# Optimization experiments

Hardware: AMD Instinct MI355X
Metric: run time of the kernel (lower is better)

## Reference

```python
import jax, jax.numpy as jnp
import numpy as np

H = 768
NH = 12
HD = H // NH


def setup_inputs() -> dict:
    key = jax.random.key(0)
    ks = jax.random.split(key, 12)
    B, S = 2, 2048
    s = 1.0 / np.sqrt(H)
    inp = {
        "hidden_states": jax.random.normal(ks[0], (B, S, H), dtype=jnp.float32),
        "attention_mask": jnp.ones((B, S), dtype=jnp.float32),
        "Wq": jax.random.normal(ks[1], (H, H), dtype=jnp.float32) * s,
        "bq": jnp.zeros((H,), dtype=jnp.float32),
        "Wk": jax.random.normal(ks[2], (H, H), dtype=jnp.float32) * s,
        "bk": jnp.zeros((H,), dtype=jnp.float32),
        "Wv": jax.random.normal(ks[3], (H, H), dtype=jnp.float32) * s,
        "bv": jnp.zeros((H,), dtype=jnp.float32),
        "Wo": jax.random.normal(ks[4], (H, H), dtype=jnp.float32) * s,
        "bo": jnp.zeros((H,), dtype=jnp.float32),
        "ln_gamma": jnp.ones((H,), dtype=jnp.float32),
        "ln_beta": jnp.zeros((H,), dtype=jnp.float32),
    }
    return inp


def _split_heads(x):
    # [B,S,H] -> [B,NH,S,HD]
    B, S, _ = x.shape
    return x.reshape(B, S, NH, HD).transpose(0, 2, 1, 3)


def reference(hidden_states, attention_mask, Wq, bq, Wk, bk, Wv, bv, Wo, bo, ln_gamma, ln_beta):
    x = hidden_states
    q = _split_heads(x @ Wq.T + bq)
    k = _split_heads(x @ Wk.T + bk)
    v = _split_heads(x @ Wv.T + bv)
    # scores: [B,NH,S,S]
    scores = jnp.einsum("bhqd,bhkd->bhqk", q, k) / jnp.sqrt(jnp.float32(HD))
    mask = (1.0 - attention_mask)[:, None, None, :] * -10000.0
    scores = scores + mask
    probs = jax.nn.softmax(scores, axis=-1)  # dropout is identity at inference
    ctx = jnp.einsum("bhqk,bhkd->bhqd", probs, v)
    B, _, S, _ = ctx.shape
    ctx = ctx.transpose(0, 2, 1, 3).reshape(B, S, H)
    out = ctx @ Wo.T + bo
    y = out + x
    mu = jnp.mean(y, axis=-1, keepdims=True)
    var = jnp.var(y, axis=-1, keepdims=True)
    y = (y - mu) / jnp.sqrt(var + 1e-5)
    return y * ln_gamma + ln_beta
```

## Files before the change

### kernel.cpp

```cpp
#include <hip/hip_runtime.h>
#include <math.h>

#define HH 768
#define NHEADS 12
#define HDIM 64
#define SEQ 2048
#define NB 2
#define L2E 1.44269504088896f

typedef __attribute__((ext_vector_type(8))) short s8v;
typedef __attribute__((ext_vector_type(4))) short s4v;
typedef __attribute__((ext_vector_type(4))) float f4v;

static __device__ inline short f2bf(float f) {
    union { float f; unsigned u; } v; v.f = f;
    unsigned r = v.u + 0x7fff + ((v.u >> 16) & 1);
    return (short)(r >> 16);
}

#if __has_builtin(__builtin_amdgcn_exp2f)
#define EXP2(x) __builtin_amdgcn_exp2f(x)
#else
#define EXP2(x) __expf((x) * 0.6931471805599453f)
#endif

__device__ __forceinline__ unsigned cvt_pk_bf16(float a, float b) {
    unsigned r;
    asm("v_cvt_pk_bf16_f32 %0, %1, %2" : "=v"(r) : "v"(a), "v"(b));
    return r;
}

__device__ __forceinline__ void gld16(const void* g, void* l) {
    __builtin_amdgcn_global_load_lds(
        (const __attribute__((address_space(1))) void*)g,
        (__attribute__((address_space(3))) void*)l, 16, 0, 0);
}

__device__ __forceinline__ int kperm(int k) {
    return (k & ~31) | (((k >> 2) & 3) << 3) | (((k >> 4) & 1) << 2) | (k & 3);
}

#define XV8   393216
#define WV8   73728
__global__ __launch_bounds__(256)
void cvt_kernel(const float* __restrict__ X, short* __restrict__ Xb,
                const float* __restrict__ W0, short* __restrict__ W0b,
                const float* __restrict__ W1, short* __restrict__ W1b,
                const float* __restrict__ W2, short* __restrict__ W2b,
                const float* __restrict__ W3, short* __restrict__ W3b)
{
    int gid = blockIdx.x * 256 + threadIdx.x;
    const float* src; short* dst; size_t off;
    if      (gid < XV8)            { src = X;  dst = Xb;  off = gid; }
    else if (gid < XV8 + WV8)      { src = W0; dst = W0b; off = gid - XV8; }
    else if (gid < XV8 + 2*WV8)    { src = W1; dst = W1b; off = gid - XV8 - WV8; }
    else if (gid < XV8 + 3*WV8)    { src = W2; dst = W2b; off = gid - XV8 - 2*WV8; }
    else if (gid < XV8 + 4*WV8)    { src = W3; dst = W3b; off = gid - XV8 - 3*WV8; }
    else return;
    off *= 8;
    float4 a = *(const float4*)(src + off);
    float4 b = *(const float4*)(src + off + 4);
    s8v o;
    o[0] = f2bf(a.x); o[1] = f2bf(a.y); o[2] = f2bf(a.z); o[3] = f2bf(a.w);
    o[4] = f2bf(b.x); o[5] = f2bf(b.y); o[6] = f2bf(b.z); o[7] = f2bf(b.w);
    *(s8v*)(dst + off) = o;
}

#define NKT (HH/32)
template<int EPI>
__global__ __launch_bounds__(256)
void gemm_mfma(const short* __restrict__ A,
               const short* __restrict__ Wq, const short* __restrict__ Wk,
               const short* __restrict__ Wv,
               const float* __restrict__ bq, const float* __restrict__ bk,
               const float* __restrict__ bv,
               short* __restrict__ Qo, short* __restrict__ Ko, short* __restrict__ Vo,
               const float* __restrict__ Xres, float* __restrict__ Fo)
{
    __shared__ __align__(16) short As[3*64*32];
    __shared__ __align__(16) short Bs[3*128*32];

    const int tid  = threadIdx.x;
    const int w    = tid >> 6;
    const int lane = tid & 63;
    const int g    = lane >> 4;
    const int r    = lane & 15;
    const int wr   = w >> 1;
    const int wc   = w & 1;

    const int NBX = (EPI == 0) ? 18 : 6;
    const int NXB = (EPI == 0) ? 144 : 48;
    const int wg  = (blockIdx.x & 7) * NXB + (blockIdx.x >> 3);
    const int bx  = wg % NBX;
    const int by  = wg / NBX;
    const int m0  = by * 64;

    int n0;
    int seg = 0;
    const short* Wb; const float* bias; short* outp; float scale;
    if (EPI == 0) {
        seg = bx / 6;
        n0 = (bx % 6) * 128;
        Wb   = seg == 0 ? Wq : seg == 1 ? Wk : Wv;
        bias = seg == 0 ? bq : seg == 1 ? bk : bv;
        outp = seg == 0 ? Qo : seg == 1 ? Ko : Vo;
        scale = seg == 0 ? (0.125f * L2E) : 1.0f;
    } else {
        n0 = bx * 128;
        Wb = Wq; bias = bq; outp = nullptr; scale = 1.0f;
    }

    const int uline = tid >> 3;
    const int us    = tid & 7;
    const int srow  = 2*uline + (us >> 2);
    const int scol  = 8 * ((us & 3) ^ (uline & 3));
    const short* Asrc  = A  + (size_t)(m0 + srow) * HH + scol;
    const short* Bsrc0 = Wb + (size_t)(n0 + srow) * HH + scol;
    const short* Bsrc1 = Wb + (size_t)(n0 + 64 + srow) * HH + scol;

    #define GSTAGE(KT, DB) do { const int k0 = (KT) * 32;                      \
        gld16(Asrc  + k0, As + (DB)*2048 + w*512);                             \
        gld16(Bsrc0 + k0, Bs + (DB)*4096 + w*512);                             \
        gld16(Bsrc1 + k0, Bs + (DB)*4096 + 2048 + w*512);                      \
    } while (0)

    f4v acc[2][4];
    #pragma unroll
    for (int i = 0; i < 2; i++)
        #pragma unroll
        for (int j = 0; j < 4; j++) acc[i][j] = (f4v){0.f,0.f,0.f,0.f};

    const int keyg = (g ^ ((r >> 1) & 3)) * 8;
    const int abase = (wr*16 + (r >> 1))*64 + (r & 1)*32 + keyg;
    const int bbase = (wc*32 + (r >> 1))*64 + (r & 1)*32 + keyg;

    #define GCOMPUTE(DB) do {                                                  \
        const short* Ab = As + (DB)*2048;                                      \
        const short* Bb = Bs + (DB)*4096;                                      \
        s8v af[2], bf[4];                                                      \
        _Pragma("unroll")                                                      \
        for (int mi = 0; mi < 2; mi++)                                         \
            af[mi] = *(const s8v*)(Ab + abase + mi*512);                       \
        _Pragma("unroll")                                                      \
        for (int ni = 0; ni < 4; ni++)                                         \
            bf[ni] = *(const s8v*)(Bb + bbase + ni*512);                       \
        __builtin_amdgcn_s_setprio(1);                                         \
        _Pragma("unroll")                                                      \
        for (int mi = 0; mi < 2; mi++)                                         \
            _Pragma("unroll")                                                  \
            for (int ni = 0; ni < 4; ni++)                                     \
                acc[mi][ni] = __builtin_amdgcn_mfma_f32_16x16x32_bf16(         \
                    af[mi], bf[ni], acc[mi][ni], 0, 0, 0);                     \
        __builtin_amdgcn_s_setprio(0);                                         \
    } while (0)

    GSTAGE(0, 0);
    GSTAGE(1, 1);

    int cur = 0, stg = 2;
    for (int kt = 0; kt < NKT - 2; ++kt) {
        GSTAGE(kt + 2, stg);
        asm volatile("s_waitcnt vmcnt(6)" ::: "memory");
        __builtin_amdgcn_s_barrier();
        GCOMPUTE(cur);
        __builtin_amdgcn_s_barrier();
        cur = (cur == 2) ? 0 : cur + 1;
        stg = (stg == 2) ? 0 : stg + 1;
    }
    asm volatile("s_waitcnt vmcnt(3)" ::: "memory");
    __builtin_amdgcn_s_barrier();
    GCOMPUTE(cur);
    cur = (cur == 2) ? 0 : cur + 1;
    asm volatile("s_waitcnt vmcnt(0)" ::: "memory");
    __builtin_amdgcn_s_barrier();
    GCOMPUTE(cur);

    if (EPI == 0) {
        if (seg < 2) {
            #pragma unroll
            for (int mi = 0; mi < 2; mi++) {
                #pragma unroll
                for (int j = 0; j < 4; j++) {
                    const int m = m0 + wr*32 + mi*16 + 4*g + j;
                    const int bb = m >> 11;
                    const int s  = m & 2047;
                    #pragma unroll
                    for (int ni = 0; ni < 4; ni++) {
                        const int n = n0 + wc*64 + ni*16 + r;
                        const int h = n >> 6;
                        const int d = n & 63;
                        outp[((size_t)((bb*NHEADS + h)*SEQ) + s)*HDIM + d] =
                            f2bf((acc[mi][ni][j] + bias[n]) * scale);
                    }
                }
            }
        } else {
            #pragma unroll
            for (int mi = 0; mi < 2; mi++) {
                const int m  = m0 + wr*32 + mi*16 + 4*g;
                const int bb = m >> 11;
                const int s  = m & 2047;
                const int sp = kperm(s);
                #pragma unroll
                for (int ni = 0; ni < 4; ni++) {
                    const int n = n0 + wc*64 + ni*16 + r;
                    const int h = n >> 6;
                    const int d = n & 63;
                    s4v pk;
                    #pragma unroll
                    for (int j = 0; j < 4; j++)
                        pk[j] = f2bf(acc[mi][ni][j] + bias[n]);
                    *(s4v*)(outp + ((size_t)((bb*NHEADS + h)*HDIM) + d)*SEQ + sp) = pk;
                }
            }
        }
    } else {
        #pragma unroll
        for (int mi = 0; mi < 2; mi++) {
            #pragma unroll
            for (int j = 0; j < 4; j++) {
                const int m = m0 + wr*32 + mi*16 + 4*g + j;
                #pragma unroll
                for (int ni = 0; ni < 4; ni++) {
                    const int n = n0 + wc*64 + ni*16 + r;
                    Fo[(size_t)m*HH + n] = acc[mi][ni][j] + bias[n] + Xres[(size_t)m*HH + n];
                }
            }
        }
    }
    #undef GSTAGE
    #undef GCOMPUTE
}

#define NPAIR (SEQ/64)
__global__ __launch_bounds__(512, 4)
void attn_mfma(const short* __restrict__ Q, const short* __restrict__ K,
               const short* __restrict__ VT, const float* __restrict__ mask,
               short* __restrict__ CTX)
{
    const int wgid = (blockIdx.x & 7) * 96 + (blockIdx.x >> 3);
    const int qt = wgid & 31;
    const int bh = wgid >> 5;
    const int h  = bh % NHEADS;
    const int b  = bh / NHEADS;

    const size_t hb = (size_t)(b * NHEADS + h);
    const short* Qg  = Q  + hb * SEQ * HDIM;
    const short* Kg  = K  + hb * SEQ * HDIM;
    const short* VTg = VT + hb * HDIM * SEQ;

    __shared__ __align__(16) char lds[40960];
    char* Kbase = lds;
    char* Vbase = lds + 16384;
    float* Mf   = (float*)(lds + 32768);

    const int tid  = threadIdx.x;
    const int w    = tid >> 6;
    const int grp  = w >> 2;
    const int wq   = w & 3;
    const int lane = tid & 63;
    const int g    = lane >> 4;
    const int r    = lane & 15;
    const int q0   = qt * 64;

    const short* qrow = Qg + (size_t)(q0 + wq*16 + r) * HDIM;
    const s8v qf0 = *(const s8v*)(qrow + 8*g);
    const s8v qf1 = *(const s8v*)(qrow + 8*g + 32);

    {
        float4 mv = *(const float4*)(mask + b*SEQ + tid*4);
        f4v md;
        md[0] = (mv.x - 1.0f) * (10000.0f * L2E);
        md[1] = (mv.y - 1.0f) * (10000.0f * L2E);
        md[2] = (mv.z - 1.0f) * (10000.0f * L2E);
        md[3] = (mv.w - 1.0f) * (10000.0f * L2E);
        *(f4v*)(Mf + kperm(tid*4)) = md;
    }

    f4v acc[4];
    #pragma unroll
    for (int t = 0; t < 4; t++) acc[t] = (f4v){0.f, 0.f, 0.f, 0.f};
    f4v accl = (f4v){0.f, 0.f, 0.f, 0.f};
    const s8v ones = (s8v){0x3F80, 0x3F80, 0x3F80, 0x3F80,
                           0x3F80, 0x3F80, 0x3F80, 0x3F80};

    const int srow = lane >> 3;
    const int scol = 8 * ((lane & 7) ^ srow);

    #define STAGE(PT, DB) do {                                                 \
        const int pk0 = (PT) * 64;                                             \
        char* kd = Kbase + (DB)*8192 + w*1024;                                 \
        gld16(Kg + (size_t)(pk0 + 8*w + srow)*HDIM + scol, kd);                \
        char* vd = Vbase + (DB)*8192 + w*1024;                                 \
        gld16(VTg + (size_t)(8*w + srow)*SEQ + pk0 + scol, vd);                \
    } while (0)

    STAGE(0, 0);
    __syncthreads();

    for (int pt = 0; pt < NPAIR; ++pt) {
        const int db = pt & 1;
        if (pt + 1 < NPAIR) STAGE(pt + 1, db ^ 1);

        const char* Kc = Kbase + db*8192 + grp*4096;
        const char* Vc = Vbase + db*8192;

        const float* mrow = Mf + pt*64 + grp*32 + 8*g;
        f4v z0 = *(const f4v*)(mrow);
        f4v z1 = *(const f4v*)(mrow + 4);

        __builtin_amdgcn_s_setprio(1);
        {
            const int sw = (r & 7) << 4;
            const char* kb0 = Kc + r * 128;
            const char* kb1 = Kc + (16 + r) * 128;
            s8v ka0 = *(const s8v*)(kb0 + ((16*g)      ^ sw));
            s8v ka1 = *(const s8v*)(kb0 + ((16*g + 64) ^ sw));
            s8v kc0 = *(const s8v*)(kb1 + ((16*g)      ^ sw));
            s8v kc1 = *(const s8v*)(kb1 + ((16*g + 64) ^ sw));
            z0 = __builtin_amdgcn_mfma_f32_16x16x32_bf16(ka0, qf0, z0, 0, 0, 0);
            z0 = __builtin_amdgcn_mfma_f32_16x16x32_bf16(ka1, qf1, z0, 0, 0, 0);
            z1 = __builtin_amdgcn_mfma_f32_16x16x32_bf16(kc0, qf0, z1, 0, 0, 0);
            z1 = __builtin_amdgcn_mfma_f32_16x16x32_bf16(kc1, qf1, z1, 0, 0, 0);
        }
        __builtin_amdgcn_s_setprio(0);

        #pragma unroll
        for (int i = 0; i < 4; i++) {
            z0[i] = EXP2(z0[i]);
            z1[i] = EXP2(z1[i]);
        }

        union { unsigned u[4]; s8v v; } pfu;
        pfu.u[0] = cvt_pk_bf16(z0[0], z0[1]);
        pfu.u[1] = cvt_pk_bf16(z0[2], z0[3]);
        pfu.u[2] = cvt_pk_bf16(z1[0], z1[1]);
        pfu.u[3] = cvt_pk_bf16(z1[2], z1[3]);
        const s8v pf = pfu.v;

        accl = __builtin_amdgcn_mfma_f32_16x16x32_bf16(pf, ones, accl, 0, 0, 0);

        __builtin_amdgcn_s_setprio(1);
        #pragma unroll
        for (int t4 = 0; t4 < 4; t4++) {
            const int vrow = 16*t4 + r;
            s8v vf = *(const s8v*)(Vc + vrow*128 + ((16*(4*grp + g)) ^ ((r & 7) << 4)));
            acc[t4] = __builtin_amdgcn_mfma_f32_16x16x32_bf16(pf, vf, acc[t4], 0, 0, 0);
        }
        __builtin_amdgcn_s_setprio(0);

        __syncthreads();
    }

    if (grp == 1) {
        float* mb = (float*)(lds + wq*5120 + lane*80);
        *(f4v*)(mb)      = acc[0];
        *(f4v*)(mb + 4)  = acc[1];
        *(f4v*)(mb + 8)  = acc[2];
        *(f4v*)(mb + 12) = acc[3];
        *(f4v*)(mb + 16) = accl;
    }
    __syncthreads();
    if (grp == 0) {
        const float* mb = (const float*)(lds + wq*5120 + lane*80);
        acc[0] += *(const f4v*)(mb);
        acc[1] += *(const f4v*)(mb + 4);
        acc[2] += *(const f4v*)(mb + 8);
        acc[3] += *(const f4v*)(mb + 12);
        accl   += *(const f4v*)(mb + 16);

        #pragma unroll
        for (int i = 0; i < 4; i++) {
            const float invl = 1.0f / accl[i];
            const size_t rowbase = ((size_t)(b*SEQ) + q0 + wq*16 + 4*g + i) * HH + h*HDIM;
            #pragma unroll
            for (int t4 = 0; t4 < 4; t4++)
                CTX[rowbase + 16*t4 + r] = f2bf(acc[t4][i] * invl);
        }
    }
    #undef STAGE
}

__global__ __launch_bounds__(256)
void ln_kernel(float* __restrict__ y, const float* __restrict__ gamma,
               const float* __restrict__ beta)
{
    const int row = blockIdx.x;
    float* p = y + (size_t)row * HH;
    const int tid = threadIdx.x;

    float v[3];
    float s = 0.f, ss = 0.f;
    #pragma unroll
    for (int i = 0; i < 3; i++) {
        float x = p[tid + i*256];
        v[i] = x;
        s += x;
        ss += x * x;
    }
    #pragma unroll
    for (int off = 32; off > 0; off >>= 1) {
        s  += __shfl_down(s,  off);
        ss += __shfl_down(ss, off);
    }
    __shared__ float sbuf[4], ssbuf[4];
    __shared__ float mu_s, rstd_s;
    const int wave = tid >> 6;
    if ((tid & 63) == 0) { sbuf[wave] = s; ssbuf[wave] = ss; }
    __syncthreads();
    if (tid == 0) {
        float S  = sbuf[0] + sbuf[1] + sbuf[2] + sbuf[3];
        float SS = ssbuf[0] + ssbuf[1] + ssbuf[2] + ssbuf[3];
        float mu = S * (1.0f / HH);
        float var = SS * (1.0f / HH) - mu * mu;
        mu_s = mu;
        rstd_s = rsqrtf(var + 1e-5f);
    }
    __syncthreads();
    const float mu = mu_s, rstd = rstd_s;
    #pragma unroll
    for (int i = 0; i < 3; i++) {
        const int c = tid + i*256;
        p[c] = (v[i] - mu) * rstd * gamma[c] + beta[c];
    }
}

extern "C" void kernel_launch(void* const* d_in, const int* in_sizes, int n_in,
                              void* d_out, int out_size, void* d_ws, size_t ws_size,
                              hipStream_t stream)
{
    const float* x     = (const float*)d_in[0];
    const float* mask  = (const float*)d_in[1];
    const float* Wq    = (const float*)d_in[2];
    const float* bq    = (const float*)d_in[3];
    const float* Wk    = (const float*)d_in[4];
    const float* bk    = (const float*)d_in[5];
    const float* Wv    = (const float*)d_in[6];
    const float* bv    = (const float*)d_in[7];
    const float* Wo    = (const float*)d_in[8];
    const float* bo    = (const float*)d_in[9];
    const float* gamma = (const float*)d_in[10];
    const float* beta  = (const float*)d_in[11];

    const size_t PER = (size_t)NB * NHEADS * SEQ * HDIM;
    const size_t WSZ = (size_t)HH * HH;
    short* wsS  = (short*)d_ws;
    short* Xb   = wsS;
    short* Wqb  = wsS + PER;
    short* Wkb  = Wqb + WSZ;
    short* Wvb  = Wkb + WSZ;
    short* Wob  = Wvb + WSZ;
    short* Qb   = Wob + WSZ;
    short* Kb   = Qb + PER;
    short* VTb  = Kb + PER;
    short* CTXb = Xb;
    float* out  = (float*)d_out;

    cvt_kernel<<<2688, 256, 0, stream>>>(x, Xb, Wq, Wqb, Wk, Wkb, Wv, Wvb, Wo, Wob);

    gemm_mfma<0><<<1152, 256, 0, stream>>>(
        Xb, Wqb, Wkb, Wvb, bq, bk, bv, Qb, Kb, VTb, nullptr, nullptr);

    attn_mfma<<<768, 512, 0, stream>>>(Qb, Kb, VTb, mask, CTXb);

    gemm_mfma<1><<<384, 256, 0, stream>>>(
        CTXb, Wob, nullptr, nullptr, bo, nullptr, nullptr,
        nullptr, nullptr, nullptr, x, out);

    ln_kernel<<<NB*SEQ, 256, 0, stream>>>(out, gamma, beta);
}
```

Baseline: 100.8 us.

## Halve output-projection tile width and switch GEMM to double buffering

The output projection GEMM now uses 64x64 tiles instead of 64x128, doubling its grid from 384 to 768 workgroups so the 256 compute units are better filled. The shared GEMM template also drops from a triple-buffered to a double-buffered LDS pipeline with one stage of prefetch, which shrinks LDS use. The QKV GEMM shares that pipeline change, so it loses a stage of load latency hiding. It also now keeps only two LDS buffers.

```diff
diff --git a/kernel.cpp b/kernel.cpp
--- a/kernel.cpp
+++ b/kernel.cpp
@@ -77,8 +77,8 @@
                short* __restrict__ Qo, short* __restrict__ Ko, short* __restrict__ Vo,
                const float* __restrict__ Xres, float* __restrict__ Fo)
 {
-    __shared__ __align__(16) short As[3*64*32];
-    __shared__ __align__(16) short Bs[3*128*32];
+    __shared__ __align__(16) short As[2*64*32];
+    __shared__ __align__(16) short Bs[2*128*32];
 
     const int tid  = threadIdx.x;
     const int w    = tid >> 6;
@@ -88,8 +88,11 @@
     const int wr   = w >> 1;
     const int wc   = w & 1;
 
-    const int NBX = (EPI == 0) ? 18 : 6;
-    const int NXB = (EPI == 0) ? 144 : 48;
+    const int NI   = (EPI == 0) ? 4 : 2;
+    const int BBUF = (EPI == 0) ? 4096 : 2048;
+
+    const int NBX = (EPI == 0) ? 18 : 12;
+    const int NXB = (EPI == 0) ? 144 : 96;
     const int wg  = (blockIdx.x & 7) * NXB + (blockIdx.x >> 3);
     const int bx  = wg % NBX;
     const int by  = wg / NBX;
@@ -106,7 +109,7 @@
         outp = seg == 0 ? Qo : seg == 1 ? Ko : Vo;
         scale = seg == 0 ? (0.125f * L2E) : 1.0f;
     } else {
-        n0 = bx * 128;
+        n0 = bx * 64;
         Wb = Wq; bias = bq; outp = nullptr; scale = 1.0f;
     }
 
@@ -116,12 +119,12 @@
     const int scol  = 8 * ((us & 3) ^ (uline & 3));
     const short* Asrc  = A  + (size_t)(m0 + srow) * HH + scol;
     const short* Bsrc0 = Wb + (size_t)(n0 + srow) * HH + scol;
-    const short* Bsrc1 = Wb + (size_t)(n0 + 64 + srow) * HH + scol;
+    const short* Bsrc1 = (EPI == 0) ? (Wb + (size_t)(n0 + 64 + srow) * HH + scol) : nullptr;
 
     #define GSTAGE(KT, DB) do { const int k0 = (KT) * 32;                      \
         gld16(Asrc  + k0, As + (DB)*2048 + w*512);                             \
-        gld16(Bsrc0 + k0, Bs + (DB)*4096 + w*512);                             \
-        gld16(Bsrc1 + k0, Bs + (DB)*4096 + 2048 + w*512);                      \
+        gld16(Bsrc0 + k0, Bs + (DB)*BBUF + w*512);                             \
+        if (EPI == 0) gld16(Bsrc1 + k0, Bs + (DB)*BBUF + 2048 + w*512);        \
     } while (0)
 
     f4v acc[2][4];
@@ -130,50 +133,45 @@
         #pragma unroll
         for (int j = 0; j < 4; j++) acc[i][j] = (f4v){0.f,0.f,0.f,0.f};
 
-    const int keyg = (g ^ ((r >> 1) & 3)) * 8;
+    const int keyg  = (g ^ ((r >> 1) & 3)) * 8;
     const int abase = (wr*16 + (r >> 1))*64 + (r & 1)*32 + keyg;
-    const int bbase = (wc*32 + (r >> 1))*64 + (r & 1)*32 + keyg;
+    const int wcl   = (EPI == 0) ? wc*32 : wc*16;
+    const int bbase = (wcl + (r >> 1))*64 + (r & 1)*32 + keyg;
 
     #define GCOMPUTE(DB) do {                                                  \
         const short* Ab = As + (DB)*2048;                                      \
-        const short* Bb = Bs + (DB)*4096;                                      \
+        const short* Bb = Bs + (DB)*BBUF;                                      \
         s8v af[2], bf[4];                                                      \
         _Pragma("unroll")                                                      \
         for (int mi = 0; mi < 2; mi++)                                         \
             af[mi] = *(const s8v*)(Ab + abase + mi*512);                       \
         _Pragma("unroll")                                                      \
-        for (int ni = 0; ni < 4; ni++)                                         \
+        for (int ni = 0; ni < NI; ni++)                                        \
             bf[ni] = *(const s8v*)(Bb + bbase + ni*512);                       \
         __builtin_amdgcn_s_setprio(1);                                         \
         _Pragma("unroll")                                                      \
         for (int mi = 0; mi < 2; mi++)                                         \
             _Pragma("unroll")                                                  \
-            for (int ni = 0; ni < 4; ni++)                                     \
+            for (int ni = 0; ni < NI; ni++)                                    \
                 acc[mi][ni] = __builtin_amdgcn_mfma_f32_16x16x32_bf16(         \
                     af[mi], bf[ni], acc[mi][ni], 0, 0, 0);                     \
         __builtin_amdgcn_s_setprio(0);                                         \
     } while (0)
 
     GSTAGE(0, 0);
-    GSTAGE(1, 1);
-
-    int cur = 0, stg = 2;
-    for (int kt = 0; kt < NKT - 2; ++kt) {
-        GSTAGE(kt + 2, stg);
-        asm volatile("s_waitcnt vmcnt(6)" ::: "memory");
+
+    for (int kt = 0; kt < NKT; ++kt) {
+        if (kt + 1 < NKT) {
+            GSTAGE(kt + 1, (kt + 1) & 1);
+            if constexpr (EPI == 0) asm volatile("s_waitcnt vmcnt(3)" ::: "memory");
+            else                    asm volatile("s_waitcnt vmcnt(2)" ::: "memory");
+        } else {
+            asm volatile("s_waitcnt vmcnt(0)" ::: "memory");
+        }
         __builtin_amdgcn_s_barrier();
-        GCOMPUTE(cur);
+        GCOMPUTE(kt & 1);
         __builtin_amdgcn_s_barrier();
-        cur = (cur == 2) ? 0 : cur + 1;
-        stg = (stg == 2) ? 0 : stg + 1;
-    }
-    asm volatile("s_waitcnt vmcnt(3)" ::: "memory");
-    __builtin_amdgcn_s_barrier();
-    GCOMPUTE(cur);
-    cur = (cur == 2) ? 0 : cur + 1;
-    asm volatile("s_waitcnt vmcnt(0)" ::: "memory");
-    __builtin_amdgcn_s_barrier();
-    GCOMPUTE(cur);
+    }
 
     if (EPI == 0) {
         if (seg < 2) {
@@ -221,8 +219,8 @@
             for (int j = 0; j < 4; j++) {
                 const int m = m0 + wr*32 + mi*16 + 4*g + j;
                 #pragma unroll
-                for (int ni = 0; ni < 4; ni++) {
-                    const int n = n0 + wc*64 + ni*16 + r;
+                for (int ni = 0; ni < 2; ni++) {
+                    const int n = n0 + wc*32 + ni*16 + r;
                     Fo[(size_t)m*HH + n] = acc[mi][ni][j] + bias[n] + Xres[(size_t)m*HH + n];
                 }
             }
@@ -463,7 +461,7 @@
 
     attn_mfma<<<768, 512, 0, stream>>>(Qb, Kb, VTb, mask, CTXb);
 
-    gemm_mfma<1><<<384, 256, 0, stream>>>(
+    gemm_mfma<1><<<768, 256, 0, stream>>>(
         CTXb, Wob, nullptr, nullptr, bo, nullptr, nullptr,
         nullptr, nullptr, nullptr, x, out);
 
```

Result: no change. 101.0 us (+0.2%).
